# Optimization experiments

Measured on AMD Instinct MI355X. Metric: run time of the kernel, lower is better.

The kernel has to match this reference:

```python
import jax, jax.numpy as jnp
import numpy as np

B, W, F, N = 256, 512, 512, 512


def setup_inputs() -> dict:
    key = jax.random.key(0)
    k1, k2, k3, k4, k5 = jax.random.split(key, 5)
    return {
        "x": jax.random.normal(k1, (B, W, F), dtype=jnp.float32),
        "weight_k": jax.random.normal(k2, (F, N), dtype=jnp.float32),
        "weight_q": jax.random.normal(k3, (F, N), dtype=jnp.float32),
        "weight_v": jax.random.normal(k4, (F, N), dtype=jnp.float32),
        "w": jax.random.normal(k5, (W, 1), dtype=jnp.float32),
    }


def reference(x, weight_k, weight_q, weight_v, w):
    # x: (B, W, F)
    n_outputs = weight_k.shape[-1]
    # Per-word K/V projections (original loops over words; here one batched GEMM)
    K = jnp.einsum("bwf,fn->bwn", x, weight_k)  # (B, W, N)
    V = jnp.einsum("bwf,fn->bwn", x, weight_v)  # (B, W, N)
    # Per-sample query: t = x^T @ w -> (F,), q = t @ weight_q -> (N,)
    t = jnp.einsum("bwf,w->bf", x, w[:, 0])     # (B, F)
    Q = t @ weight_q                              # (B, N)
    # Scores over words, scaled, softmax across the word axis
    scores = jnp.einsum("bn,bwn->bw", Q, K) / jnp.sqrt(jnp.float32(n_outputs))
    weights = jax.nn.softmax(scores, axis=1)      # (B, W)
    # Weighted sum of V over words
    return jnp.einsum("bw,bwn->bn", weights, V)   # (B, N)
```

## Files before the change

kernel.cpp:

```cpp
#include <hip/hip_runtime.h>
#include <math.h>

#define B 256
#define W 512
#define F 512
#define N 512
#define GPART 4
#define WPG (W / GPART)

__global__ __launch_bounds__(512) void tpart_kernel(
    const float* __restrict__ x,
    const float* __restrict__ wvec,
    float* __restrict__ t_part)
{
    const int blk = blockIdx.x;
    const int g   = blk & (GPART - 1);
    const int b   = blk >> 2;
    const int tid = threadIdx.x;
    const int ws  = tid >> 7;
    const int f4  = tid & 127;

    __shared__ float s_w[WPG];
    __shared__ float s_part[4][F];

    if (tid < WPG) s_w[tid] = wvec[g * WPG + tid];
    __syncthreads();

    const float* xb = x + (size_t)b * W * F + (size_t)(g * WPG + ws * 32) * F;
    float4 acc = make_float4(0.f, 0.f, 0.f, 0.f);
#pragma unroll 8
    for (int i = 0; i < 32; ++i) {
        const float4 xv = *(const float4*)(xb + (size_t)i * F + f4 * 4);
        const float  ww = s_w[ws * 32 + i];
        acc.x += xv.x * ww; acc.y += xv.y * ww;
        acc.z += xv.z * ww; acc.w += xv.w * ww;
    }
    *(float4*)&s_part[ws][f4 * 4] = acc;
    __syncthreads();

    const float t = (s_part[0][tid] + s_part[1][tid])
                  + (s_part[2][tid] + s_part[3][tid]);
    t_part[(size_t)blk * F + tid] = t;
}

__global__ __launch_bounds__(512) void qr_kernel(
    const float* __restrict__ t_part,
    const float* __restrict__ Wq,
    const float* __restrict__ Wk,
    float* __restrict__ r_out)
{
    __shared__ float s_t[F];
    __shared__ float s_q[N];
    const int b = blockIdx.x, tid = threadIdx.x;

    float t = 0.f;
#pragma unroll
    for (int g = 0; g < GPART; ++g)
        t += t_part[((size_t)b * GPART + g) * F + tid];
    s_t[tid] = t;
    __syncthreads();

    float q0 = 0.f, q1 = 0.f, q2 = 0.f, q3 = 0.f;
#pragma unroll 4
    for (int f = 0; f < F; f += 4) {
        q0 += s_t[f + 0] * Wq[(size_t)(f + 0) * N + tid];
        q1 += s_t[f + 1] * Wq[(size_t)(f + 1) * N + tid];
        q2 += s_t[f + 2] * Wq[(size_t)(f + 2) * N + tid];
        q3 += s_t[f + 3] * Wq[(size_t)(f + 3) * N + tid];
    }
    s_q[tid] = (q0 + q1) + (q2 + q3);
    __syncthreads();

    const float4* wkrow = (const float4*)(Wk + (size_t)tid * N);
    float r0 = 0.f, r1 = 0.f, r2 = 0.f, r3 = 0.f;
#pragma unroll 8
    for (int n4 = 0; n4 < N / 4; ++n4) {
        const float4 kv = wkrow[n4];
        const float4 qv = *(const float4*)&s_q[n4 * 4];
        r0 += kv.x * qv.x; r1 += kv.y * qv.y;
        r2 += kv.z * qv.z; r3 += kv.w * qv.w;
    }
    r_out[(size_t)b * F + tid] =
        ((r0 + r1) + (r2 + r3)) * 0.04419417382415922f;
}

__global__ __launch_bounds__(512) void attn_kernel(
    const float* __restrict__ x,
    const float* __restrict__ Wv,
    const float* __restrict__ r_in,
    float* __restrict__ out)
{
    const int b    = blockIdx.x;
    const int tid  = threadIdx.x;
    const int lane = tid & 63;
    const int wv   = tid >> 6;

    __shared__ float s_c[8][F];
    __shared__ float s_m[8];
    __shared__ float s_l[8];
    __shared__ float s_cf[F];

    const float* xb = x + (size_t)b * W * F;
    const float* rb = r_in + (size_t)b * F;
    const float4 r0 = *(const float4*)(rb + lane * 4);
    const float4 r1 = *(const float4*)(rb + 256 + lane * 4);

    float m = -INFINITY, l = 0.f;
    float4 c0 = make_float4(0.f, 0.f, 0.f, 0.f);
    float4 c1 = make_float4(0.f, 0.f, 0.f, 0.f);

#pragma unroll 2
    for (int i = 0; i < 64; i += 2) {
        const float* rowA = xb + (size_t)(wv * 64 + i) * F;
        const float* rowB = rowA + F;
        const float4 a0 = *(const float4*)(rowA + lane * 4);
        const float4 a1 = *(const float4*)(rowA + 256 + lane * 4);
        const float4 b0 = *(const float4*)(rowB + lane * 4);
        const float4 b1 = *(const float4*)(rowB + 256 + lane * 4);

        float dA = a0.x * r0.x + a0.y * r0.y + a0.z * r0.z + a0.w * r0.w
                 + a1.x * r1.x + a1.y * r1.y + a1.z * r1.z + a1.w * r1.w;
        float dB = b0.x * r0.x + b0.y * r0.y + b0.z * r0.z + b0.w * r0.w
                 + b1.x * r1.x + b1.y * r1.y + b1.z * r1.z + b1.w * r1.w;
#pragma unroll
        for (int off = 32; off >= 1; off >>= 1) {
            dA += __shfl_xor(dA, off, 64);
            dB += __shfl_xor(dB, off, 64);
        }

        float mn = fmaxf(m, dA);
        float sc = __expf(m - mn);
        float p  = __expf(dA - mn);
        l = l * sc + p;
        c0.x = c0.x * sc + p * a0.x; c0.y = c0.y * sc + p * a0.y;
        c0.z = c0.z * sc + p * a0.z; c0.w = c0.w * sc + p * a0.w;
        c1.x = c1.x * sc + p * a1.x; c1.y = c1.y * sc + p * a1.y;
        c1.z = c1.z * sc + p * a1.z; c1.w = c1.w * sc + p * a1.w;
        m = mn;

        mn = fmaxf(m, dB);
        sc = __expf(m - mn);
        p  = __expf(dB - mn);
        l = l * sc + p;
        c0.x = c0.x * sc + p * b0.x; c0.y = c0.y * sc + p * b0.y;
        c0.z = c0.z * sc + p * b0.z; c0.w = c0.w * sc + p * b0.w;
        c1.x = c1.x * sc + p * b1.x; c1.y = c1.y * sc + p * b1.y;
        c1.z = c1.z * sc + p * b1.z; c1.w = c1.w * sc + p * b1.w;
        m = mn;
    }

    *(float4*)&s_c[wv][lane * 4]       = c0;
    *(float4*)&s_c[wv][256 + lane * 4] = c1;
    if (lane == 0) { s_m[wv] = m; s_l[wv] = l; }
    __syncthreads();

    float M = -INFINITY;
#pragma unroll
    for (int j = 0; j < 8; ++j) M = fmaxf(M, s_m[j]);
    float L = 0.f;
    float alpha[8];
#pragma unroll
    for (int j = 0; j < 8; ++j) {
        alpha[j] = __expf(s_m[j] - M);
        L += alpha[j] * s_l[j];
    }
    const float invL = 1.f / L;

    float cf = 0.f;
#pragma unroll
    for (int j = 0; j < 8; ++j) cf += alpha[j] * s_c[j][tid];
    s_cf[tid] = cf * invL;
    __syncthreads();

    float o0 = 0.f, o1 = 0.f, o2 = 0.f, o3 = 0.f;
#pragma unroll 4
    for (int f = 0; f < F; f += 4) {
        o0 += s_cf[f + 0] * Wv[(size_t)(f + 0) * N + tid];
        o1 += s_cf[f + 1] * Wv[(size_t)(f + 1) * N + tid];
        o2 += s_cf[f + 2] * Wv[(size_t)(f + 2) * N + tid];
        o3 += s_cf[f + 3] * Wv[(size_t)(f + 3) * N + tid];
    }
    out[(size_t)b * N + tid] = (o0 + o1) + (o2 + o3);
}

extern "C" void kernel_launch(void* const* d_in, const int* in_sizes, int n_in,
                              void* d_out, int out_size, void* d_ws, size_t ws_size,
                              hipStream_t stream)
{
    const float* x    = (const float*)d_in[0];
    const float* Wk   = (const float*)d_in[1];
    const float* Wq   = (const float*)d_in[2];
    const float* Wv   = (const float*)d_in[3];
    const float* wvec = (const float*)d_in[4];
    float* out    = (float*)d_out;
    float* t_part = (float*)d_ws;
    float* r      = t_part + (size_t)B * GPART * F;

    tpart_kernel<<<B * GPART, 512, 0, stream>>>(x, wvec, t_part);
    qr_kernel<<<B, 512, 0, stream>>>(t_part, Wq, Wk, r);
    attn_kernel<<<B, 512, 0, stream>>>(x, Wv, r, out);
}
```

Before: 465.5 us.

## Split attention over word groups with a separate combine kernel

The attention pass is split into eight word-group blocks per batch. Each block computes a partial online-softmax state (max, sum, weighted x row) and writes it to workspace, and a new combine kernel merges the partials and applies the Wv projection. The t-partial kernel also moves to eight groups of 256-thread blocks, and the Wq/Wv GEMV loops use eight accumulators. This targets the low parallelism of 256 large blocks streaming 256MB of x; the cost is one extra launch and extra workspace traffic.

```diff
diff --git a/kernel.cpp b/kernel.cpp
--- a/kernel.cpp
+++ b/kernel.cpp
@@ -5,42 +5,41 @@
 #define W 512
 #define F 512
 #define N 512
-#define GPART 4
-#define WPG (W / GPART)
-
-__global__ __launch_bounds__(512) void tpart_kernel(
+#define GP 8
+#define WPB (W / GP)
+
+__global__ __launch_bounds__(256, 8) void tpart_kernel(
     const float* __restrict__ x,
     const float* __restrict__ wvec,
     float* __restrict__ t_part)
 {
-    const int blk = blockIdx.x;
-    const int g   = blk & (GPART - 1);
-    const int b   = blk >> 2;
-    const int tid = threadIdx.x;
-    const int ws  = tid >> 7;
-    const int f4  = tid & 127;
-
-    __shared__ float s_w[WPG];
-    __shared__ float s_part[4][F];
-
-    if (tid < WPG) s_w[tid] = wvec[g * WPG + tid];
-    __syncthreads();
-
-    const float* xb = x + (size_t)b * W * F + (size_t)(g * WPG + ws * 32) * F;
+    const int blk  = blockIdx.x;
+    const int g    = blk & (GP - 1);
+    const int b    = blk >> 3;
+    const int tid  = threadIdx.x;
+    const int half = tid >> 7;
+    const int f4   = tid & 127;
+
+    __shared__ float s_w[WPB];
+    __shared__ float s_part[2][F];
+
+    if (tid < WPB) s_w[tid] = wvec[g * WPB + tid];
+    __syncthreads();
+
+    const float* xb = x + (size_t)b * W * F + (size_t)(g * WPB + half * 32) * F;
     float4 acc = make_float4(0.f, 0.f, 0.f, 0.f);
 #pragma unroll 8
     for (int i = 0; i < 32; ++i) {
         const float4 xv = *(const float4*)(xb + (size_t)i * F + f4 * 4);
-        const float  ww = s_w[ws * 32 + i];
+        const float  ww = s_w[half * 32 + i];
         acc.x += xv.x * ww; acc.y += xv.y * ww;
         acc.z += xv.z * ww; acc.w += xv.w * ww;
     }
-    *(float4*)&s_part[ws][f4 * 4] = acc;
-    __syncthreads();
-
-    const float t = (s_part[0][tid] + s_part[1][tid])
-                  + (s_part[2][tid] + s_part[3][tid]);
-    t_part[(size_t)blk * F + tid] = t;
+    *(float4*)&s_part[half][f4 * 4] = acc;
+    __syncthreads();
+
+    t_part[(size_t)blk * F + tid]       = s_part[0][tid]       + s_part[1][tid];
+    t_part[(size_t)blk * F + tid + 256] = s_part[0][tid + 256] + s_part[1][tid + 256];
 }
 
 __global__ __launch_bounds__(512) void qr_kernel(
@@ -55,20 +54,20 @@
 
     float t = 0.f;
 #pragma unroll
-    for (int g = 0; g < GPART; ++g)
-        t += t_part[((size_t)b * GPART + g) * F + tid];
+    for (int g = 0; g < GP; ++g)
+        t += t_part[((size_t)b * GP + g) * F + tid];
     s_t[tid] = t;
     __syncthreads();
 
-    float q0 = 0.f, q1 = 0.f, q2 = 0.f, q3 = 0.f;
+    float qa[8] = {0.f, 0.f, 0.f, 0.f, 0.f, 0.f, 0.f, 0.f};
 #pragma unroll 4
-    for (int f = 0; f < F; f += 4) {
-        q0 += s_t[f + 0] * Wq[(size_t)(f + 0) * N + tid];
-        q1 += s_t[f + 1] * Wq[(size_t)(f + 1) * N + tid];
-        q2 += s_t[f + 2] * Wq[(size_t)(f + 2) * N + tid];
-        q3 += s_t[f + 3] * Wq[(size_t)(f + 3) * N + tid];
-    }
-    s_q[tid] = (q0 + q1) + (q2 + q3);
+    for (int f = 0; f < F; f += 8) {
+#pragma unroll
+        for (int j = 0; j < 8; ++j)
+            qa[j] += s_t[f + j] * Wq[(size_t)(f + j) * N + tid];
+    }
+    s_q[tid] = ((qa[0] + qa[1]) + (qa[2] + qa[3]))
+             + ((qa[4] + qa[5]) + (qa[6] + qa[7]));
     __syncthreads();
 
     const float4* wkrow = (const float4*)(Wk + (size_t)tid * N);
@@ -84,21 +83,22 @@
         ((r0 + r1) + (r2 + r3)) * 0.04419417382415922f;
 }
 
-__global__ __launch_bounds__(512) void attn_kernel(
+__global__ __launch_bounds__(256, 6) void attn_part_kernel(
     const float* __restrict__ x,
-    const float* __restrict__ Wv,
     const float* __restrict__ r_in,
-    float* __restrict__ out)
-{
-    const int b    = blockIdx.x;
+    float* __restrict__ c_part,
+    float* __restrict__ ml_part)
+{
+    const int blk  = blockIdx.x;
+    const int g    = blk & (GP - 1);
+    const int b    = blk >> 3;
     const int tid  = threadIdx.x;
     const int lane = tid & 63;
     const int wv   = tid >> 6;
 
-    __shared__ float s_c[8][F];
-    __shared__ float s_m[8];
-    __shared__ float s_l[8];
-    __shared__ float s_cf[F];
+    __shared__ float s_c[4][F];
+    __shared__ float s_m[4];
+    __shared__ float s_l[4];
 
     const float* xb = x + (size_t)b * W * F;
     const float* rb = r_in + (size_t)b * F;
@@ -109,9 +109,10 @@
     float4 c0 = make_float4(0.f, 0.f, 0.f, 0.f);
     float4 c1 = make_float4(0.f, 0.f, 0.f, 0.f);
 
+    const int wbase = g * WPB + wv * 16;
 #pragma unroll 2
-    for (int i = 0; i < 64; i += 2) {
-        const float* rowA = xb + (size_t)(wv * 64 + i) * F;
+    for (int i = 0; i < 16; i += 2) {
+        const float* rowA = xb + (size_t)(wbase + i) * F;
         const float* rowB = rowA + F;
         const float4 a0 = *(const float4*)(rowA + lane * 4);
         const float4 a1 = *(const float4*)(rowA + 256 + lane * 4);
@@ -154,33 +155,61 @@
     if (lane == 0) { s_m[wv] = m; s_l[wv] = l; }
     __syncthreads();
 
+    float M = fmaxf(fmaxf(s_m[0], s_m[1]), fmaxf(s_m[2], s_m[3]));
+    float a0w = __expf(s_m[0] - M), a1w = __expf(s_m[1] - M);
+    float a2w = __expf(s_m[2] - M), a3w = __expf(s_m[3] - M);
+    float L = a0w * s_l[0] + a1w * s_l[1] + a2w * s_l[2] + a3w * s_l[3];
+
+#pragma unroll
+    for (int k = 0; k < 2; ++k) {
+        const int f = tid + k * 256;
+        c_part[(size_t)blk * F + f] =
+            a0w * s_c[0][f] + a1w * s_c[1][f] + a2w * s_c[2][f] + a3w * s_c[3][f];
+    }
+    if (tid == 0) { ml_part[blk * 2] = M; ml_part[blk * 2 + 1] = L; }
+}
+
+__global__ __launch_bounds__(512) void combine_kernel(
+    const float* __restrict__ c_part,
+    const float* __restrict__ ml_part,
+    const float* __restrict__ Wv,
+    float* __restrict__ out)
+{
+    __shared__ float s_cf[F];
+    const int b = blockIdx.x, tid = threadIdx.x;
+
+    float Mg[GP];
+#pragma unroll
+    for (int g = 0; g < GP; ++g) Mg[g] = ml_part[(b * GP + g) * 2];
     float M = -INFINITY;
 #pragma unroll
-    for (int j = 0; j < 8; ++j) M = fmaxf(M, s_m[j]);
+    for (int g = 0; g < GP; ++g) M = fmaxf(M, Mg[g]);
+
     float L = 0.f;
-    float alpha[8];
-#pragma unroll
-    for (int j = 0; j < 8; ++j) {
-        alpha[j] = __expf(s_m[j] - M);
-        L += alpha[j] * s_l[j];
+    float alpha[GP];
+#pragma unroll
+    for (int g = 0; g < GP; ++g) {
+        alpha[g] = __expf(Mg[g] - M);
+        L += alpha[g] * ml_part[(b * GP + g) * 2 + 1];
     }
     const float invL = 1.f / L;
 
     float cf = 0.f;
 #pragma unroll
-    for (int j = 0; j < 8; ++j) cf += alpha[j] * s_c[j][tid];
+    for (int g = 0; g < GP; ++g)
+        cf += alpha[g] * c_part[((size_t)b * GP + g) * F + tid];
     s_cf[tid] = cf * invL;
     __syncthreads();
 
-    float o0 = 0.f, o1 = 0.f, o2 = 0.f, o3 = 0.f;
+    float oa[8] = {0.f, 0.f, 0.f, 0.f, 0.f, 0.f, 0.f, 0.f};
 #pragma unroll 4
-    for (int f = 0; f < F; f += 4) {
-        o0 += s_cf[f + 0] * Wv[(size_t)(f + 0) * N + tid];
-        o1 += s_cf[f + 1] * Wv[(size_t)(f + 1) * N + tid];
-        o2 += s_cf[f + 2] * Wv[(size_t)(f + 2) * N + tid];
-        o3 += s_cf[f + 3] * Wv[(size_t)(f + 3) * N + tid];
-    }
-    out[(size_t)b * N + tid] = (o0 + o1) + (o2 + o3);
+    for (int f = 0; f < F; f += 8) {
+#pragma unroll
+        for (int j = 0; j < 8; ++j)
+            oa[j] += s_cf[f + j] * Wv[(size_t)(f + j) * N + tid];
+    }
+    out[(size_t)b * N + tid] = ((oa[0] + oa[1]) + (oa[2] + oa[3]))
+                             + ((oa[4] + oa[5]) + (oa[6] + oa[7]));
 }
 
 extern "C" void kernel_launch(void* const* d_in, const int* in_sizes, int n_in,
@@ -192,11 +221,14 @@
     const float* Wq   = (const float*)d_in[2];
     const float* Wv   = (const float*)d_in[3];
     const float* wvec = (const float*)d_in[4];
-    float* out    = (float*)d_out;
-    float* t_part = (float*)d_ws;
-    float* r      = t_part + (size_t)B * GPART * F;
-
-    tpart_kernel<<<B * GPART, 512, 0, stream>>>(x, wvec, t_part);
+    float* out     = (float*)d_out;
+    float* t_part  = (float*)d_ws;
+    float* r       = t_part + (size_t)B * GP * F;
+    float* c_part  = r + (size_t)B * F;
+    float* ml_part = c_part + (size_t)B * GP * F;
+
+    tpart_kernel<<<B * GP, 256, 0, stream>>>(x, wvec, t_part);
     qr_kernel<<<B, 512, 0, stream>>>(t_part, Wq, Wk, r);
-    attn_kernel<<<B, 512, 0, stream>>>(x, Wv, r, out);
-}
+    attn_part_kernel<<<B * GP, 256, 0, stream>>>(x, r, c_part, ml_part);
+    combine_kernel<<<B, 512, 0, stream>>>(c_part, ml_part, Wv, out);
+}
```

Result: slower. 491.8 us (+5.7%).
